# Kernel optimization log

Measured on AMD Instinct MI355X. Metric: run time of the kernel, lower is better.

## Reference

```python
import jax, jax.numpy as jnp
import numpy as np

N_NET = 32
N_UNITS = 2048
N_EXC = int(N_UNITS * 0.8)   # 1638
N_INH = N_UNITS - N_EXC      # 410
TAU = 0.1
DT = 0.01
CONN_P = 0.1
INHIB_STRENGTH = 1.0
GAUSS_SIGMA = 2.0


def _local_weights(key, n_pre, n_post, is_excitatory):
    k1, k2 = jax.random.split(key)
    mask = (jax.random.uniform(k1, (N_NET, n_pre, n_post)) < CONN_P).astype(jnp.float32)
    w = jax.random.normal(k2, (N_NET, n_pre, n_post), dtype=jnp.float32) * mask
    if is_excitatory:
        return jnp.maximum(w, 0.0)
    return -jnp.abs(w)


def setup_inputs() -> dict:
    key = jax.random.key(0)
    ks = jax.random.split(key, 8)
    unit_input = jax.random.normal(ks[0], (N_NET, N_UNITS), dtype=jnp.float32)
    r = jax.random.uniform(ks[1], (N_NET, N_UNITS), dtype=jnp.float32)
    W_ee = _local_weights(ks[2], N_EXC, N_EXC, True)
    W_ei = _local_weights(ks[3], N_EXC, N_INH, True)
    W_ie = _local_weights(ks[4], N_INH, N_EXC, False)
    W_ii = _local_weights(ks[5], N_INH, N_INH, False)
    # Gaussian-tuned inter-network inhibition, zero diagonal, sparse mask
    pos = jnp.arange(N_NET, dtype=jnp.float32)
    dist = pos[:, None] - pos[None, :]
    g = -INHIB_STRENGTH * jnp.exp(-0.5 * (dist / GAUSS_SIGMA) ** 2)
    g = g * (1.0 - jnp.eye(N_NET, dtype=jnp.float32))
    mask = (jax.random.uniform(ks[6], (N_NET, N_NET, N_INH, N_INH)) < CONN_P).astype(jnp.float32)
    W_inter = g[:, :, None, None] * mask
    return {"unit_input": unit_input, "r": r, "W_ee": W_ee, "W_ei": W_ei,
            "W_ie": W_ie, "W_ii": W_ii, "W_inter": W_inter}


def reference(unit_input, r, W_ee, W_ei, W_ie, W_ii, W_inter):
    # r: [N, U] state; split excitatory / inhibitory
    r_e = r[:, :N_EXC]   # [N, E]
    r_i = r[:, N_EXC:]   # [N, I]
    # Faithful to source: inhibition onto network i uses network i's OWN
    # inhibitory rates (local_net.r), summed over all j != i (diag(W_inter)=0).
    # inh[i, a] = sum_j sum_b W_inter[i, j, a, b] * r_i[i, b]
    inter_inh = jnp.einsum('ijab,ib->ia', W_inter, r_i)  # [N, I]
    in_e = unit_input[:, :N_EXC]
    in_i = unit_input[:, N_EXC:] + inter_inh
    # per-network matvecs: W.T @ r  -> einsum over presynaptic axis
    input_e = jnp.einsum('npq,np->nq', W_ee, r_e) + jnp.einsum('npq,np->nq', W_ie, r_i) + in_e
    input_i = jnp.einsum('npq,np->nq', W_ei, r_e) + jnp.einsum('npq,np->nq', W_ii, r_i) + in_i
    total = jnp.concatenate([input_e, input_i], axis=1)  # [N, U]
    phi = jax.nn.relu(total)
    r_new = r + DT * ((-r + phi) / TAU)  # Euler step
    return r_new  # [N, U] unit-level rates (return_unit_outputs=True)
```

## Files before the change

kernel.cpp:

```cpp
#include <hip/hip_runtime.h>

#define NNET 32
#define NUNITS 2048
#define NEXC 1638
#define NINH 410

__device__ __forceinline__ void col_matvec(const float* __restrict__ W,
                                           const float* __restrict__ r,
                                           float* __restrict__ acc,
                                           int rel_blk,
                                           int P, int Q, int QB, int PB, int PCH,
                                           int qoff, int vecoff) {
    int n   = rel_blk / (QB * PB);
    int rem = rel_blk % (QB * PB);
    int qb  = rem / PB;
    int pb  = rem % PB;

    int q  = qb * 256 + threadIdx.x;
    int p0 = pb * PCH;
    int p1 = min(p0 + PCH, P);
    int len = p1 - p0;

    __shared__ float s_r[256];
    if ((int)threadIdx.x < len)
        s_r[threadIdx.x] = r[n * NUNITS + vecoff + p0 + threadIdx.x];
    __syncthreads();

    if (q >= Q) return;

    const float* Wp = W + ((size_t)n * P + p0) * Q + q;
    float a = 0.f;
    int p = 0;
    for (; p + 4 <= len; p += 4) {
        float w0 = Wp[(size_t)(p + 0) * Q];
        float w1 = Wp[(size_t)(p + 1) * Q];
        float w2 = Wp[(size_t)(p + 2) * Q];
        float w3 = Wp[(size_t)(p + 3) * Q];
        a += w0 * s_r[p] + w1 * s_r[p + 1] + w2 * s_r[p + 2] + w3 * s_r[p + 3];
    }
    for (; p < len; ++p)
        a += Wp[(size_t)p * Q] * s_r[p];

    atomicAdd(&acc[n * NUNITS + qoff + q], a);
}

__device__ __forceinline__ void inter_job(const float* __restrict__ Wint,
                                          const float* __restrict__ r,
                                          float* __restrict__ acc,
                                          int rel_blk) {
    int i  = rel_blk / 103;
    int ab = rel_blk % 103;

    __shared__ float s_ri[NINH];
    for (int t = threadIdx.x; t < NINH; t += 256)
        s_ri[t] = r[i * NUNITS + NEXC + t];
    __syncthreads();

    int wave = threadIdx.x >> 6;
    int lane = threadIdx.x & 63;
    int a = ab * 4 + wave;
    if (a >= NINH) return;

    const float* base = Wint + ((size_t)i * NNET * NINH + a) * NINH;
    float accv = 0.f;
    for (int j = 0; j < NNET; ++j) {
        const float* row = base + (size_t)j * NINH * NINH;
        const float2* row2 = (const float2*)row;
        for (int b2 = lane; b2 < NINH / 2; b2 += 64) {
            float2 w = row2[b2];
            accv += w.x * s_ri[2 * b2] + w.y * s_ri[2 * b2 + 1];
        }
    }
    for (int off = 32; off; off >>= 1)
        accv += __shfl_down(accv, off, 64);
    if (lane == 0)
        atomicAdd(&acc[i * NUNITS + NEXC + a], accv);
}

__global__ __launch_bounds__(256) void fused_matvec(
    const float* __restrict__ Wee, const float* __restrict__ Wei,
    const float* __restrict__ Wie, const float* __restrict__ Wii,
    const float* __restrict__ Wint,
    const float* __restrict__ r, float* __restrict__ acc) {
    int blk = blockIdx.x;
    if (blk < 1792) {
        col_matvec(Wee, r, acc, blk,        1638, 1638, 7, 8, 205, 0,    0);
    } else if (blk < 2240) {
        col_matvec(Wie, r, acc, blk - 1792,  410, 1638, 7, 2, 205, 0,    NEXC);
    } else if (blk < 2752) {
        col_matvec(Wei, r, acc, blk - 2240, 1638,  410, 2, 8, 205, NEXC, 0);
    } else if (blk < 2880) {
        col_matvec(Wii, r, acc, blk - 2752,  410,  410, 2, 2, 205, NEXC, NEXC);
    } else {
        inter_job(Wint, r, acc, blk - 2880);
    }
}

__global__ __launch_bounds__(256) void finalize_kernel(
    const float* __restrict__ r, const float* __restrict__ uin,
    const float* __restrict__ acc, float* __restrict__ out) {
    int idx = blockIdx.x * 256 + threadIdx.x;
    if (idx < NNET * NUNITS) {
        float total = acc[idx] + uin[idx];
        float phi = fmaxf(total, 0.f);
        out[idx] = 0.9f * r[idx] + 0.1f * phi;
    }
}

extern "C" void kernel_launch(void* const* d_in, const int* in_sizes, int n_in,
                              void* d_out, int out_size, void* d_ws, size_t ws_size,
                              hipStream_t stream) {
    const float* unit_input = (const float*)d_in[0];
    const float* r          = (const float*)d_in[1];
    const float* W_ee       = (const float*)d_in[2];
    const float* W_ei       = (const float*)d_in[3];
    const float* W_ie       = (const float*)d_in[4];
    const float* W_ii       = (const float*)d_in[5];
    const float* W_inter    = (const float*)d_in[6];
    float* out = (float*)d_out;
    float* acc = (float*)d_ws;

    hipMemsetAsync(acc, 0, NNET * NUNITS * sizeof(float), stream);

    fused_matvec<<<6176, 256, 0, stream>>>(W_ee, W_ei, W_ie, W_ii, W_inter, r, acc);

    finalize_kernel<<<(NNET * NUNITS + 255) / 256, 256, 0, stream>>>(r, unit_input, acc, out);
}
```

Baseline: 1.183 ms.

## Vectorize column matvec loads to float2 and split inter-inhibition work per (i,j) plane

The column matvecs now give each thread two adjacent output columns and load the weights as float2, which halves the block count for the local weight matrices. The inter-network term is regrouped so each block handles one (i, j) plane half of W_inter and streams contiguous rows, with one atomic per row instead of one per accumulated row across all j. The aim is wider, more coalesced loads on a bandwidth-bound workload and better locality for the large W_inter tensor. In exchange there are more atomics on the inhibitory accumulators and fewer blocks for the local matvecs.

```diff
diff --git a/kernel.cpp b/kernel.cpp
--- a/kernel.cpp
+++ b/kernel.cpp
@@ -5,21 +5,20 @@
 #define NEXC 1638
 #define NINH 410
 
-__device__ __forceinline__ void col_matvec(const float* __restrict__ W,
-                                           const float* __restrict__ r,
-                                           float* __restrict__ acc,
-                                           int rel_blk,
-                                           int P, int Q, int QB, int PB, int PCH,
-                                           int qoff, int vecoff) {
+__device__ __forceinline__ void col_matvec2(const float* __restrict__ W,
+                                            const float* __restrict__ r,
+                                            float* __restrict__ acc,
+                                            int rel_blk,
+                                            int P, int Q, int QB, int PB, int PCH,
+                                            int qoff, int vecoff) {
     int n   = rel_blk / (QB * PB);
     int rem = rel_blk % (QB * PB);
     int qb  = rem / PB;
     int pb  = rem % PB;
 
-    int q  = qb * 256 + threadIdx.x;
+    int q  = qb * 512 + 2 * (int)threadIdx.x;
     int p0 = pb * PCH;
-    int p1 = min(p0 + PCH, P);
-    int len = p1 - p0;
+    int len = min(PCH, P - p0);
 
     __shared__ float s_r[256];
     if ((int)threadIdx.x < len)
@@ -28,28 +27,35 @@
 
     if (q >= Q) return;
 
-    const float* Wp = W + ((size_t)n * P + p0) * Q + q;
-    float a = 0.f;
+    const float2* Wp  = (const float2*)(W + ((size_t)n * P + p0) * Q + q);
+    size_t       step = (size_t)(Q >> 1);
+    float ax = 0.f, ay = 0.f;
     int p = 0;
     for (; p + 4 <= len; p += 4) {
-        float w0 = Wp[(size_t)(p + 0) * Q];
-        float w1 = Wp[(size_t)(p + 1) * Q];
-        float w2 = Wp[(size_t)(p + 2) * Q];
-        float w3 = Wp[(size_t)(p + 3) * Q];
-        a += w0 * s_r[p] + w1 * s_r[p + 1] + w2 * s_r[p + 2] + w3 * s_r[p + 3];
+        float2 w0 = Wp[(size_t)(p + 0) * step];
+        float2 w1 = Wp[(size_t)(p + 1) * step];
+        float2 w2 = Wp[(size_t)(p + 2) * step];
+        float2 w3 = Wp[(size_t)(p + 3) * step];
+        ax += w0.x * s_r[p] + w1.x * s_r[p + 1] + w2.x * s_r[p + 2] + w3.x * s_r[p + 3];
+        ay += w0.y * s_r[p] + w1.y * s_r[p + 1] + w2.y * s_r[p + 2] + w3.y * s_r[p + 3];
     }
-    for (; p < len; ++p)
-        a += Wp[(size_t)p * Q] * s_r[p];
+    for (; p < len; ++p) {
+        float2 w = Wp[(size_t)p * step];
+        ax += w.x * s_r[p];
+        ay += w.y * s_r[p];
+    }
 
-    atomicAdd(&acc[n * NUNITS + qoff + q], a);
+    atomicAdd(&acc[n * NUNITS + qoff + q],     ax);
+    atomicAdd(&acc[n * NUNITS + qoff + q + 1], ay);
 }
 
-__device__ __forceinline__ void inter_job(const float* __restrict__ Wint,
-                                          const float* __restrict__ r,
-                                          float* __restrict__ acc,
-                                          int rel_blk) {
-    int i  = rel_blk / 103;
-    int ab = rel_blk % 103;
+__device__ __forceinline__ void inter_ij(const float* __restrict__ Wint,
+                                         const float* __restrict__ r,
+                                         float* __restrict__ acc,
+                                         int rel_blk) {
+    int i    = rel_blk >> 6;
+    int j    = (rel_blk >> 1) & 31;
+    int half = rel_blk & 1;
 
     __shared__ float s_ri[NINH];
     for (int t = threadIdx.x; t < NINH; t += 256)
@@ -58,23 +64,22 @@
 
     int wave = threadIdx.x >> 6;
     int lane = threadIdx.x & 63;
-    int a = ab * 4 + wave;
-    if (a >= NINH) return;
 
-    const float* base = Wint + ((size_t)i * NNET * NINH + a) * NINH;
-    float accv = 0.f;
-    for (int j = 0; j < NNET; ++j) {
-        const float* row = base + (size_t)j * NINH * NINH;
-        const float2* row2 = (const float2*)row;
+    const float* plane = Wint + (size_t)(i * NNET + j) * NINH * NINH;
+    int a0 = half * 205;
+    int a1 = a0 + 205;
+    for (int a = a0 + wave; a < a1; a += 4) {
+        const float2* row2 = (const float2*)(plane + (size_t)a * NINH);
+        float s = 0.f;
         for (int b2 = lane; b2 < NINH / 2; b2 += 64) {
             float2 w = row2[b2];
-            accv += w.x * s_ri[2 * b2] + w.y * s_ri[2 * b2 + 1];
+            s += w.x * s_ri[2 * b2] + w.y * s_ri[2 * b2 + 1];
         }
+        for (int off = 32; off; off >>= 1)
+            s += __shfl_down(s, off, 64);
+        if (lane == 0)
+            atomicAdd(&acc[i * NUNITS + NEXC + a], s);
     }
-    for (int off = 32; off; off >>= 1)
-        accv += __shfl_down(accv, off, 64);
-    if (lane == 0)
-        atomicAdd(&acc[i * NUNITS + NEXC + a], accv);
 }
 
 __global__ __launch_bounds__(256) void fused_matvec(
@@ -83,16 +88,16 @@
     const float* __restrict__ Wint,
     const float* __restrict__ r, float* __restrict__ acc) {
     int blk = blockIdx.x;
-    if (blk < 1792) {
-        col_matvec(Wee, r, acc, blk,        1638, 1638, 7, 8, 205, 0,    0);
-    } else if (blk < 2240) {
-        col_matvec(Wie, r, acc, blk - 1792,  410, 1638, 7, 2, 205, 0,    NEXC);
-    } else if (blk < 2752) {
-        col_matvec(Wei, r, acc, blk - 2240, 1638,  410, 2, 8, 205, NEXC, 0);
-    } else if (blk < 2880) {
-        col_matvec(Wii, r, acc, blk - 2752,  410,  410, 2, 2, 205, NEXC, NEXC);
+    if (blk < 1024) {
+        col_matvec2(Wee, r, acc, blk,        1638, 1638, 4, 8, 205, 0,    0);
+    } else if (blk < 1280) {
+        col_matvec2(Wie, r, acc, blk - 1024,  410, 1638, 4, 2, 205, 0,    NEXC);
+    } else if (blk < 1536) {
+        col_matvec2(Wei, r, acc, blk - 1280, 1638,  410, 1, 8, 205, NEXC, 0);
+    } else if (blk < 1600) {
+        col_matvec2(Wii, r, acc, blk - 1536,  410,  410, 1, 2, 205, NEXC, NEXC);
     } else {
-        inter_job(Wint, r, acc, blk - 2880);
+        inter_ij(Wint, r, acc, blk - 1600);
     }
 }
 
@@ -122,7 +127,7 @@
 
     hipMemsetAsync(acc, 0, NNET * NUNITS * sizeof(float), stream);
 
-    fused_matvec<<<6176, 256, 0, stream>>>(W_ee, W_ei, W_ie, W_ii, W_inter, r, acc);
+    fused_matvec<<<3648, 256, 0, stream>>>(W_ee, W_ei, W_ie, W_ii, W_inter, r, acc);
 
     finalize_kernel<<<(NNET * NUNITS + 255) / 256, 256, 0, stream>>>(r, unit_input, acc, out);
 }
```

After: 1.217 ms. 2.9% more time.
